# Kernel optimization log

Hardware: AMD Instinct MI355X
Metric: run time of the kernel (lower is better)

The kernel has to match this reference:

```python
import jax, jax.numpy as jnp
import numpy as np

BS, T, D, H = 2500, 400, 16, 32  # nodes(batch), time steps, input_dim, hidden_dim


def _xavier(key, shape):
    fan_in, fan_out = shape[0], shape[1]
    lim = np.sqrt(6.0 / (fan_in + fan_out)).astype(np.float32)
    return jax.random.uniform(key, shape, jnp.float32, -lim, lim)


def setup_inputs() -> dict:
    key = jax.random.key(0)
    ks = jax.random.split(key, 6)
    x = jax.random.normal(ks[0], (BS, T, D), jnp.float32)
    # dense adjacency over the batch/node dim, scaled small like a normalized river-network adjacency
    adj = jax.random.normal(ks[1], (BS, BS), jnp.float32) * 0.01
    return {
        "x": x,
        "adj": adj,
        "W_ih": _xavier(ks[2], (D, 4 * H)),
        "W_hh": _xavier(ks[3], (H, 4 * H)),
        "b": jnp.zeros((4 * H,), jnp.float32),
        "W_q": _xavier(ks[4], (H, H)),
        "b_q": jnp.zeros((H,), jnp.float32),
        "W_d": _xavier(ks[5], (H, 1)),
        "b_d": jnp.zeros((1,), jnp.float32),
    }


def reference(x, adj, W_ih, W_hh, b, W_q, b_q, W_d, b_d):
    # RGCN_Multi.forward_task0 (eval mode: dropouts are identity).
    HS = W_q.shape[0]
    bs = x.shape[0]

    def step(carry, x_t):
        h, c = carry  # [bs, HS] each
        gates = x_t @ W_ih + h @ W_hh + b  # [bs, 4*HS]
        i_t = jax.nn.sigmoid(gates[:, :HS])
        f_t = jax.nn.sigmoid(gates[:, HS:2 * HS])
        g_t = jnp.tanh(gates[:, 2 * HS:3 * HS])
        o_t = jax.nn.sigmoid(gates[:, 3 * HS:])
        q_t = jnp.tanh(h @ W_q + b_q)          # [bs, HS]
        c = f_t * (c + adj @ q_t) + i_t * g_t  # graph aggregation fused into cell state
        h = o_t * jnp.tanh(c)
        return (h, c), h

    h0 = jnp.zeros((bs, HS), x.dtype)
    (_, _), hs = jax.lax.scan(step, (h0, h0), jnp.swapaxes(x, 0, 1))  # hs: [T, bs, HS]
    hidden_seq = jnp.swapaxes(hs, 0, 1)  # [bs, T, HS]
    return hidden_seq @ W_d + b_d        # Task0Module dense head -> [bs, T, 1]
```

## Files before the change

### kernel.cpp

```cpp
#include <hip/hip_runtime.h>
#include <hip/hip_bf16.h>

#define BSN   2500
#define TT    400
#define DIN   16
#define HS    32
#define G4    128
#define NBLK  157
#define NTHR  512
#define ROWS  16
#define MPAD  (NBLK * ROWS)
#define KPAD  2528
#define NCHUNK 79
#define ADJW  2536
#define HPAD  36
#define FLAGSTRIDE 16

#define REGUS   (NCHUNK * 512)

#define WS_FLAGS_OFF  0
#define WS_ADJ_OFF    16384
#define WS_ADJ_BYTES  ((size_t)MPAD * KPAD * 2)
#define WS_QT_OFF     (WS_ADJ_OFF + WS_ADJ_BYTES)
#define QT_SLICE      ((size_t)HS * KPAD)
#define WS_NEED_RING  (WS_QT_OFF + (size_t)TT * QT_SLICE * 2)

typedef __attribute__((ext_vector_type(8))) __bf16 bf16x8;
typedef __attribute__((ext_vector_type(4))) float floatx4;
typedef unsigned short ushort_t;
typedef unsigned long long u64_t;

__device__ __forceinline__ float sigmoid_fast(float v) {
    return 1.0f / (1.0f + __expf(-v));
}
__device__ __forceinline__ float tanh_fast(float v) {
    float e = __expf(2.0f * v);
    return 1.0f - 2.0f / (e + 1.0f);
}
__device__ __forceinline__ ushort_t f2bf(float f) {
    union { float f; unsigned u; } x; x.f = f;
    unsigned r = x.u + 0x7fffu + ((x.u >> 16) & 1u);
    return (ushort_t)(r >> 16);
}

__global__ void sentinel(float* __restrict__ out, int n) {
    int i = blockIdx.x * blockDim.x + threadIdx.x;
    if (i < n) out[i] = 12345.0f;
}

__global__ void prep(const float* __restrict__ adj, ushort_t* __restrict__ adj_bf,
                     ushort_t* __restrict__ qT, unsigned* __restrict__ flags) {
    const size_t idx0 = (size_t)blockIdx.x * blockDim.x + threadIdx.x;
    const size_t stride = (size_t)gridDim.x * blockDim.x;
    const size_t total = (size_t)MPAD * KPAD;
    for (size_t idx = idx0; idx < total; idx += stride) {
        int r = (int)(idx / KPAD);
        int k = (int)(idx - (size_t)r * KPAD);
        float v = (r < BSN && k < BSN) ? adj[(size_t)r * BSN + k] : 0.0f;
        adj_bf[idx] = f2bf(v);
    }
    for (size_t idx = idx0; idx < 2 * QT_SLICE; idx += stride) qT[idx] = 0;
    if (idx0 < NBLK * FLAGSTRIDE) flags[idx0] = 0;
}

#define QLOAD(p) __hip_atomic_load((p), __ATOMIC_RELAXED, __HIP_MEMORY_SCOPE_AGENT)

template<int NC>
__device__ __forceinline__ void p2_frag(const ushort_t* __restrict__ arow,
                                        const ushort_t* __restrict__ q0,
                                        const ushort_t* __restrict__ q1,
                                        const int cbeg,
                                        floatx4& acc0, floatx4& acc1) {
    bf16x8 b0[NC], b1[NC];
#pragma unroll
    for (int i = 0; i < NC; i++) {
        b0[i] = *(const bf16x8*)(q0 + (size_t)(cbeg + i) * 512);
        b1[i] = *(const bf16x8*)(q1 + (size_t)(cbeg + i) * 512);
    }
#pragma unroll
    for (int i = 0; i < NC; i++) {
        bf16x8 av = *(const bf16x8*)(arow + (cbeg + i) * 32);
        acc0 = __builtin_amdgcn_mfma_f32_16x16x32_bf16(av, b0[i], acc0, 0, 0, 0);
        acc1 = __builtin_amdgcn_mfma_f32_16x16x32_bf16(av, b1[i], acc1, 0, 0, 0);
    }
}

template<bool RING>
__global__ void __launch_bounds__(NTHR, 2) rgcn_main(
    const float* __restrict__ x,
    const float* __restrict__ W_ih,
    const float* __restrict__ W_hh,
    const float* __restrict__ bias,
    const float* __restrict__ W_q,
    const float* __restrict__ b_q,
    const float* __restrict__ W_d,
    const float* __restrict__ b_d,
    const ushort_t* __restrict__ adj_bf,
    ushort_t* __restrict__ qT,
    unsigned* __restrict__ flags,
    float* __restrict__ out)
{
    const int tid  = threadIdx.x;
    const int blk  = blockIdx.x;
    const int base = blk * ROWS;
    const int wv   = tid >> 6;
    const int lane = tid & 63;

    __shared__ __align__(16) ushort_t adj_lds[ROWS * ADJW];
    __shared__ __align__(16) float x_lds[ROWS][DIN];
    __shared__ __align__(16) float h_lds[ROWS][HPAD];
    __shared__ __align__(16) float c_lds[ROWS][HPAD];
    __shared__ __align__(16) float q_lds[ROWS][HPAD];
    __shared__ __align__(16) float wq_lds[HS][HS];
    __shared__ __align__(16) float out_lds[ROWS][16];
    __shared__ float gates_lds[ROWS][G4];
    __shared__ float part[2][7][2][16][16];

    const int u2 = tid & 63;
    float wih0[DIN], wih1[DIN], whh0[HS], whh1[HS];
#pragma unroll
    for (int k = 0; k < DIN; k++) {
        wih0[k] = W_ih[k*G4 + u2]; wih1[k] = W_ih[k*G4 + u2 + 64];
        asm volatile("" : "+v"(wih0[k]), "+v"(wih1[k]));
    }
#pragma unroll
    for (int k = 0; k < HS; k++) {
        whh0[k] = W_hh[k*G4 + u2]; whh1[k] = W_hh[k*G4 + u2 + 64];
        asm volatile("" : "+v"(whh0[k]), "+v"(whh1[k]));
    }
    const float bu0 = bias[u2], bu1 = bias[u2 + 64];

    const int hq = tid & 31;
    const int nq = tid >> 5;
    const float bqv = b_q[hq];
    const float wdv = W_d[hq];
    const float bdv = b_d[0];
    float c_reg = 0.0f;

    int cbeg = 0, nch = 0;
    if (wv >= 1 && wv <= 3)      { cbeg = (wv - 1) * 12;      nch = 12; }
    else if (wv >= 4 && wv <= 6) { cbeg = 36 + (wv - 4) * 11; nch = 11; }
    else if (wv == 7)            { cbeg = 69;                 nch = 10; }
    const int pollbase = 2 * cbeg;
    const int pollcnt  = (wv == 0) ? 0
                       : ((2 * (cbeg + nch) < NBLK ? 2 * (cbeg + nch) : NBLK) - pollbase);
    const unsigned* pollf = flags + (size_t)(pollbase + lane) * FLAGSTRIDE;
    const bool dopoll = (wv >= 1) && (lane < pollcnt);

    int xnode = -1, xk = lane & 15;
    if (wv >= 1 && lane < 32)                   xnode = 2*wv + (lane >> 4);
    else if ((wv == 1 || wv == 2) && lane < 48) xnode = wv - 1;
    const int xgn = base + xnode;
    const bool xok = (xnode >= 0) && (xgn < BSN);

    {
        const int n16_per_row = KPAD / 8;
        for (int i = tid; i < ROWS * n16_per_row; i += NTHR) {
            int r = i / n16_per_row, o = i - r * n16_per_row;
            ((uint4*)(adj_lds + r * ADJW))[o] =
                ((const uint4*)(adj_bf + (size_t)(base + r) * KPAD))[o];
        }
    }
    for (int i = tid; i < HS * HS; i += NTHR) (&wq_lds[0][0])[i] = W_q[i];
    for (int i = tid; i < ROWS * HPAD; i += NTHR) {
        (&h_lds[0][0])[i] = 0.0f;
        (&c_lds[0][0])[i] = 0.0f;
    }
    __syncthreads();

    auto do_gates = [&](int nn) {
        float a0 = bu0, a1 = bu1;
#pragma unroll
        for (int k4 = 0; k4 < DIN/4; k4++) {
            float4 xv = *(const float4*)&x_lds[nn][k4*4];
            a0 = fmaf(xv.x, wih0[k4*4+0], a0); a1 = fmaf(xv.x, wih1[k4*4+0], a1);
            a0 = fmaf(xv.y, wih0[k4*4+1], a0); a1 = fmaf(xv.y, wih1[k4*4+1], a1);
            a0 = fmaf(xv.z, wih0[k4*4+2], a0); a1 = fmaf(xv.z, wih1[k4*4+2], a1);
            a0 = fmaf(xv.w, wih0[k4*4+3], a0); a1 = fmaf(xv.w, wih1[k4*4+3], a1);
        }
#pragma unroll
        for (int k4 = 0; k4 < HS/4; k4++) {
            float4 hv = *(const float4*)&h_lds[nn][k4*4];
            a0 = fmaf(hv.x, whh0[k4*4+0], a0); a1 = fmaf(hv.x, whh1[k4*4+0], a1);
            a0 = fmaf(hv.y, whh0[k4*4+1], a0); a1 = fmaf(hv.y, whh1[k4*4+1], a1);
            a0 = fmaf(hv.z, whh0[k4*4+2], a0); a1 = fmaf(hv.z, whh1[k4*4+2], a1);
            a0 = fmaf(hv.w, whh0[k4*4+3], a0); a1 = fmaf(hv.w, whh1[k4*4+3], a1);
        }
        gates_lds[nn][u2]      = sigmoid_fast(a0);
        gates_lds[nn][u2 + 64] = (u2 < HS) ? tanh_fast(a1) : sigmoid_fast(a1);
    };

    if constexpr (RING) {
        float xreg = xok ? x[(size_t)xgn * (TT*DIN) + xk] : 0.0f;

        const int pc    = blk >> 1;
        const int phalf = blk & 1;
        const int preg  = lane >> 5;
        const int pidx  = lane & 31;
        const int ph    = (pidx & 15) + 16 * preg;
        const int pln0  = (pidx >> 4) * 8;

        for (int t = 0; t < TT; t++) {
            const unsigned phase = (unsigned)(t + 1);
            const ushort_t* qslice = qT + (size_t)t * QT_SLICE;

            {
                float a = bqv;
#pragma unroll
                for (int k4 = 0; k4 < HS/4; k4++) {
                    float4 hv = *(const float4*)&h_lds[nq][k4*4];
                    a = fmaf(hv.x, wq_lds[k4*4+0][hq], a);
                    a = fmaf(hv.y, wq_lds[k4*4+1][hq], a);
                    a = fmaf(hv.z, wq_lds[k4*4+2][hq], a);
                    a = fmaf(hv.w, wq_lds[k4*4+3][hq], a);
                }
                q_lds[nq][hq] = tanh_fast(a);
            }
            __syncthreads();

            if (wv == 0) {
                unsigned d[4];
#pragma unroll
                for (int j = 0; j < 4; j++) {
                    const int n0 = pln0 + 2*j;
                    d[j] = (unsigned)f2bf(q_lds[n0][ph])
                         | ((unsigned)f2bf(q_lds[n0 + 1][ph]) << 16);
                }
                u64_t v0 = (u64_t)d[0] | ((u64_t)d[1] << 32);
                u64_t v1 = (u64_t)d[2] | ((u64_t)d[3] << 32);
                u64_t* dst = (u64_t*)((ushort_t*)qslice + (size_t)preg * REGUS
                                      + (size_t)pc * 512 + phalf * 256 + pidx * 8);
                __hip_atomic_store(dst,     v0, __ATOMIC_RELAXED, __HIP_MEMORY_SCOPE_AGENT);
                __hip_atomic_store(dst + 1, v1, __ATOMIC_RELAXED, __HIP_MEMORY_SCOPE_AGENT);
                asm volatile("s_waitcnt vmcnt(0)" ::: "memory");
                if (lane == 0) {
                    __hip_atomic_store(flags + blk * FLAGSTRIDE, phase,
                                       __ATOMIC_RELAXED, __HIP_MEMORY_SCOPE_AGENT);
                }
            } else {
                if (xnode >= 0) {
                    x_lds[xnode][xk] = xok ? xreg : 0.0f;
                    const int tn = (t + 1 < TT) ? (t + 1) : (TT - 1);
                    if (xok) xreg = x[(size_t)xgn * (TT*DIN) + (size_t)tn * DIN + xk];
                }
                do_gates(2*wv);
                do_gates(2*wv + 1);
                if (wv <= 2) do_gates(wv - 1);
            }

            if (dopoll) {
                while (QLOAD(pollf) < phase) {}
            }

            if (wv >= 1) {
                floatx4 acc0 = {0.f,0.f,0.f,0.f}, acc1 = {0.f,0.f,0.f,0.f};
                const int mcol = lane & 15;
                const int kb   = lane >> 4;
                const ushort_t* arow = adj_lds + mcol * ADJW + kb*8;
                const ushort_t* q0 = qslice + (size_t)lane * 8;
                const ushort_t* q1 = qslice + (size_t)REGUS + (size_t)lane * 8;
                if (wv <= 3)      p2_frag<12>(arow, q0, q1, cbeg, acc0, acc1);
                else if (wv <= 6) p2_frag<11>(arow, q0, q1, cbeg, acc0, acc1);
                else              p2_frag<10>(arow, q0, q1, cbeg, acc0, acc1);
#pragma unroll
                for (int r = 0; r < 4; r++) {
                    part[t & 1][wv - 1][0][kb*4 + r][mcol] = acc0[r];
                    part[t & 1][wv - 1][1][kb*4 + r][mcol] = acc1[r];
                }
            }
            __syncthreads();

            {
                const int ntile = hq >> 4, col = hq & 15;
                float agg = 0.0f;
#pragma unroll
                for (int j = 0; j < 7; j++) agg += part[t & 1][j][ntile][nq][col];
                float iv = gates_lds[nq][hq];
                float fv = gates_lds[nq][HS + hq];
                float gv = gates_lds[nq][2*HS + hq];
                float ov = gates_lds[nq][3*HS + hq];
                float cv = fv * (c_reg + agg) + iv * gv;
                float hvv = ov * tanh_fast(cv);
                c_reg = cv;
                h_lds[nq][hq] = hvv;
                float p = hvv * wdv;
                p += __shfl_xor(p, 16);
                p += __shfl_xor(p, 8);
                p += __shfl_xor(p, 4);
                p += __shfl_xor(p, 2);
                p += __shfl_xor(p, 1);
                if (hq == 0) out_lds[nq][t & 15] = p + bdv;
            }

            if ((t & 15) == 15) {
                __syncthreads();
                if (wv == 7) {
                    const int node = lane >> 2, qtr = lane & 3;
                    const int gn = base + node;
                    if (gn < BSN) {
                        *(float4*)(out + (size_t)gn * TT + (t - 15) + qtr * 4) =
                            *(const float4*)&out_lds[node][qtr * 4];
                    }
                }
            }
        }
    } else {
        for (int t = 0; t < TT; t++) {
            const unsigned phase = (unsigned)(t + 1);
            ushort_t* qbuf = qT + (size_t)(t & 1) * QT_SLICE;

            {
                float a = bqv;
#pragma unroll
                for (int k4 = 0; k4 < HS/4; k4++) {
                    float4 hv = *(const float4*)&h_lds[nq][k4*4];
                    a = fmaf(hv.x, wq_lds[k4*4+0][hq], a);
                    a = fmaf(hv.y, wq_lds[k4*4+1][hq], a);
                    a = fmaf(hv.z, wq_lds[k4*4+2][hq], a);
                    a = fmaf(hv.w, wq_lds[k4*4+3][hq], a);
                }
                q_lds[nq][hq] = tanh_fast(a);
            }
            __syncthreads();

            if (tid < 256) {
                const int h0 = tid >> 3;
                const int pr = tid & 7;
                unsigned val = (unsigned)f2bf(q_lds[2*pr][h0])
                             | ((unsigned)f2bf(q_lds[2*pr + 1][h0]) << 16);
                unsigned* p = (unsigned*)(qbuf + (size_t)h0 * KPAD + base) + pr;
                __hip_atomic_store(p, val, __ATOMIC_RELAXED, __HIP_MEMORY_SCOPE_AGENT);
            }
            if (lane < 32) {
                const int node = 2*wv + (lane >> 4), k = lane & 15;
                const int gn = base + node;
                x_lds[node][k] = (gn < BSN) ? x[(size_t)gn * (TT*DIN) + (size_t)t*DIN + k] : 0.0f;
            }
            do_gates(2*wv);
            do_gates(2*wv + 1);
            asm volatile("s_waitcnt vmcnt(0)" ::: "memory");
            __syncthreads();
            if (tid == 0) {
                __hip_atomic_store(flags + blk * FLAGSTRIDE, phase,
                                   __ATOMIC_RELAXED, __HIP_MEMORY_SCOPE_AGENT);
            }
            if (tid < NBLK) {
                const unsigned* f = flags + tid * FLAGSTRIDE;
                while (QLOAD(f) < phase) {}
            }
            __syncthreads();

            {
                floatx4 acc0 = {0.f,0.f,0.f,0.f}, acc1 = {0.f,0.f,0.f,0.f};
                const int mcol = lane & 15;
                const int kb   = lane >> 4;
                const ushort_t* arow = adj_lds + mcol * ADJW + kb*8;
                const u64_t* q0 = (const u64_t*)(qbuf + (size_t)mcol        * KPAD) + kb*2;
                const u64_t* q1 = (const u64_t*)(qbuf + (size_t)(mcol + 16) * KPAD) + kb*2;
                const int cb2 = wv * 10;
                const int ce2 = (cb2 + 10 < NCHUNK) ? cb2 + 10 : NCHUNK;
                for (int c = cb2; c < ce2; c++) {
                    bf16x8 av = *(const bf16x8*)(arow + c*32);
                    union { u64_t u[2]; bf16x8 v; } b0, b1;
                    b0.u[0] = QLOAD(q0 + c*8);
                    b0.u[1] = QLOAD(q0 + c*8 + 1);
                    b1.u[0] = QLOAD(q1 + c*8);
                    b1.u[1] = QLOAD(q1 + c*8 + 1);
                    acc0 = __builtin_amdgcn_mfma_f32_16x16x32_bf16(av, b0.v, acc0, 0, 0, 0);
                    acc1 = __builtin_amdgcn_mfma_f32_16x16x32_bf16(av, b1.v, acc1, 0, 0, 0);
                }
                part[wv >> 2][(wv & 3) + ((wv >> 2) ? 3 : 0)][0][kb*4 + 0][mcol] = acc0[0];
#pragma unroll
                for (int r = 0; r < 4; r++) {
                    part[0][wv % 7][0][kb*4 + r][mcol] = 0.0f;
                }
                float* pw = &part[0][0][0][0][0] + (size_t)wv * 2 * 16 * 16;
#pragma unroll
                for (int r = 0; r < 4; r++) {
                    pw[(0*16 + kb*4 + r) * 16 + mcol] = acc0[r];
                    pw[(1*16 + kb*4 + r) * 16 + mcol] = acc1[r];
                }
            }
            __syncthreads();

            {
                const int ntile = hq >> 4, col = hq & 15;
                float agg = 0.0f;
                const float* pbase = &part[0][0][0][0][0];
#pragma unroll
                for (int w = 0; w < 8; w++) {
                    agg += pbase[(size_t)w * 2 * 16 * 16 + (ntile*16 + nq) * 16 + col];
                }
                float iv = gates_lds[nq][hq];
                float fv = gates_lds[nq][HS + hq];
                float gv = gates_lds[nq][2*HS + hq];
                float ov = gates_lds[nq][3*HS + hq];
                float cv = fv * (c_lds[nq][hq] + agg) + iv * gv;
                float hv = ov * tanh_fast(cv);
                c_lds[nq][hq] = cv;
                h_lds[nq][hq] = hv;
                float p = hv * wdv;
                p += __shfl_xor(p, 16);
                p += __shfl_xor(p, 8);
                p += __shfl_xor(p, 4);
                p += __shfl_xor(p, 2);
                p += __shfl_xor(p, 1);
                if (hq == 0) {
                    int gn = base + nq;
                    if (gn < BSN) out[(size_t)gn * TT + t] = p + bdv;
                }
            }
            __syncthreads();
        }
    }
}

extern "C" void kernel_launch(void* const* d_in, const int* in_sizes, int n_in,
                              void* d_out, int out_size, void* d_ws, size_t ws_size,
                              hipStream_t stream) {
    const float* x    = (const float*)d_in[0];
    const float* adj  = (const float*)d_in[1];
    const float* W_ih = (const float*)d_in[2];
    const float* W_hh = (const float*)d_in[3];
    const float* bias = (const float*)d_in[4];
    const float* W_q  = (const float*)d_in[5];
    const float* b_q  = (const float*)d_in[6];
    const float* W_d  = (const float*)d_in[7];
    const float* b_d  = (const float*)d_in[8];
    float* out = (float*)d_out;

    unsigned* flags = (unsigned*)((char*)d_ws + WS_FLAGS_OFF);
    ushort_t* adj_bf = (ushort_t*)((char*)d_ws + WS_ADJ_OFF);
    ushort_t* qT = (ushort_t*)((char*)d_ws + WS_QT_OFF);

    const bool ring = (ws_size >= WS_NEED_RING);

    hipLaunchKernelGGL(sentinel, dim3((out_size + 255) / 256), dim3(256), 0, stream,
                       out, out_size);
    hipLaunchKernelGGL(prep, dim3(2048), dim3(256), 0, stream, adj, adj_bf, qT, flags);

    const ushort_t* adj_bf_c = adj_bf;
    void* args[] = {
        (void*)&x, (void*)&W_ih, (void*)&W_hh, (void*)&bias, (void*)&W_q,
        (void*)&b_q, (void*)&W_d, (void*)&b_d, (void*)&adj_bf_c, (void*)&qT,
        (void*)&flags, (void*)&out
    };
    if (ring) {
        hipLaunchCooperativeKernel((void*)&rgcn_main<true>, dim3(NBLK), dim3(NTHR),
                                   args, 0, stream);
    } else {
        hipLaunchCooperativeKernel((void*)&rgcn_main<false>, dim3(NBLK), dim3(NTHR),
                                   args, 0, stream);
    }
}
```

Measured before the change: 1.831 ms.

## Store adjacency in MFMA fragment order, keep W_q in registers, move output flush

Rearranges the per-block adjacency tile in LDS into fragment-contiguous order, so each lane reads its bf16x8 operand from a contiguous 512-element chunk without a padded row stride. W_q columns are loaded into per-thread registers instead of LDS, removing LDS reads from the q projection. The periodic output flush moves from a separate barrier-guarded step at t%16==15 into the wave-0 idle slot at the next 16-step boundary, which drops one __syncthreads per 16 steps. Register pressure rises by 32 floats per thread under a 2-blocks-per-CU launch bound.

```diff
diff --git a/kernel.cpp b/kernel.cpp
--- a/kernel.cpp
+++ b/kernel.cpp
@@ -12,7 +12,6 @@
 #define MPAD  (NBLK * ROWS)
 #define KPAD  2528
 #define NCHUNK 79
-#define ADJW  2536
 #define HPAD  36
 #define FLAGSTRIDE 16
 
@@ -66,7 +65,7 @@
 #define QLOAD(p) __hip_atomic_load((p), __ATOMIC_RELAXED, __HIP_MEMORY_SCOPE_AGENT)
 
 template<int NC>
-__device__ __forceinline__ void p2_frag(const ushort_t* __restrict__ arow,
+__device__ __forceinline__ void p2_frag(const ushort_t* __restrict__ afrag,
                                         const ushort_t* __restrict__ q0,
                                         const ushort_t* __restrict__ q1,
                                         const int cbeg,
@@ -79,7 +78,7 @@
     }
 #pragma unroll
     for (int i = 0; i < NC; i++) {
-        bf16x8 av = *(const bf16x8*)(arow + (cbeg + i) * 32);
+        bf16x8 av = *(const bf16x8*)(afrag + (size_t)(cbeg + i) * 512);
         acc0 = __builtin_amdgcn_mfma_f32_16x16x32_bf16(av, b0[i], acc0, 0, 0, 0);
         acc1 = __builtin_amdgcn_mfma_f32_16x16x32_bf16(av, b1[i], acc1, 0, 0, 0);
     }
@@ -106,12 +105,11 @@
     const int wv   = tid >> 6;
     const int lane = tid & 63;
 
-    __shared__ __align__(16) ushort_t adj_lds[ROWS * ADJW];
+    __shared__ __align__(16) ushort_t adj_lds[NCHUNK * 512];
     __shared__ __align__(16) float x_lds[ROWS][DIN];
     __shared__ __align__(16) float h_lds[ROWS][HPAD];
     __shared__ __align__(16) float c_lds[ROWS][HPAD];
     __shared__ __align__(16) float q_lds[ROWS][HPAD];
-    __shared__ __align__(16) float wq_lds[HS][HS];
     __shared__ __align__(16) float out_lds[ROWS][16];
     __shared__ float gates_lds[ROWS][G4];
     __shared__ float part[2][7][2][16][16];
@@ -136,6 +134,13 @@
     const float wdv = W_d[hq];
     const float bdv = b_d[0];
     float c_reg = 0.0f;
+
+    float wqr[HS];
+#pragma unroll
+    for (int k = 0; k < HS; k++) {
+        wqr[k] = W_q[k*HS + hq];
+        asm volatile("" : "+v"(wqr[k]));
+    }
 
     int cbeg = 0, nch = 0;
     if (wv >= 1 && wv <= 3)      { cbeg = (wv - 1) * 12;      nch = 12; }
@@ -157,11 +162,11 @@
         const int n16_per_row = KPAD / 8;
         for (int i = tid; i < ROWS * n16_per_row; i += NTHR) {
             int r = i / n16_per_row, o = i - r * n16_per_row;
-            ((uint4*)(adj_lds + r * ADJW))[o] =
+            int c = o >> 2, kb = o & 3;
+            *(uint4*)(adj_lds + (size_t)c * 512 + (size_t)(kb * 16 + r) * 8) =
                 ((const uint4*)(adj_bf + (size_t)(base + r) * KPAD))[o];
         }
     }
-    for (int i = tid; i < HS * HS; i += NTHR) (&wq_lds[0][0])[i] = W_q[i];
     for (int i = tid; i < ROWS * HPAD; i += NTHR) {
         (&h_lds[0][0])[i] = 0.0f;
         (&c_lds[0][0])[i] = 0.0f;
@@ -190,6 +195,19 @@
         gates_lds[nn][u2 + 64] = (u2 < HS) ? tanh_fast(a1) : sigmoid_fast(a1);
     };
 
+    auto do_p1b = [&]() {
+        float a = bqv;
+#pragma unroll
+        for (int k4 = 0; k4 < HS/4; k4++) {
+            float4 hv = *(const float4*)&h_lds[nq][k4*4];
+            a = fmaf(hv.x, wqr[k4*4+0], a);
+            a = fmaf(hv.y, wqr[k4*4+1], a);
+            a = fmaf(hv.z, wqr[k4*4+2], a);
+            a = fmaf(hv.w, wqr[k4*4+3], a);
+        }
+        q_lds[nq][hq] = tanh_fast(a);
+    };
+
     if constexpr (RING) {
         float xreg = xok ? x[(size_t)xgn * (TT*DIN) + xk] : 0.0f;
 
@@ -204,18 +222,7 @@
             const unsigned phase = (unsigned)(t + 1);
             const ushort_t* qslice = qT + (size_t)t * QT_SLICE;
 
-            {
-                float a = bqv;
-#pragma unroll
-                for (int k4 = 0; k4 < HS/4; k4++) {
-                    float4 hv = *(const float4*)&h_lds[nq][k4*4];
-                    a = fmaf(hv.x, wq_lds[k4*4+0][hq], a);
-                    a = fmaf(hv.y, wq_lds[k4*4+1][hq], a);
-                    a = fmaf(hv.z, wq_lds[k4*4+2][hq], a);
-                    a = fmaf(hv.w, wq_lds[k4*4+3][hq], a);
-                }
-                q_lds[nq][hq] = tanh_fast(a);
-            }
+            do_p1b();
             __syncthreads();
 
             if (wv == 0) {
@@ -237,6 +244,14 @@
                     __hip_atomic_store(flags + blk * FLAGSTRIDE, phase,
                                        __ATOMIC_RELAXED, __HIP_MEMORY_SCOPE_AGENT);
                 }
+                if (t >= 16 && (t & 15) == 0) {
+                    const int node = lane >> 2, qtr = lane & 3;
+                    const int gn = base + node;
+                    if (gn < BSN) {
+                        *(float4*)(out + (size_t)gn * TT + (t - 16) + qtr * 4) =
+                            *(const float4*)&out_lds[node][qtr * 4];
+                    }
+                }
             } else {
                 if (xnode >= 0) {
                     x_lds[xnode][xk] = xok ? xreg : 0.0f;
@@ -256,12 +271,12 @@
                 floatx4 acc0 = {0.f,0.f,0.f,0.f}, acc1 = {0.f,0.f,0.f,0.f};
                 const int mcol = lane & 15;
                 const int kb   = lane >> 4;
-                const ushort_t* arow = adj_lds + mcol * ADJW + kb*8;
+                const ushort_t* afrag = adj_lds + (size_t)lane * 8;
                 const ushort_t* q0 = qslice + (size_t)lane * 8;
                 const ushort_t* q1 = qslice + (size_t)REGUS + (size_t)lane * 8;
-                if (wv <= 3)      p2_frag<12>(arow, q0, q1, cbeg, acc0, acc1);
-                else if (wv <= 6) p2_frag<11>(arow, q0, q1, cbeg, acc0, acc1);
-                else              p2_frag<10>(arow, q0, q1, cbeg, acc0, acc1);
+                if (wv <= 3)      p2_frag<12>(afrag, q0, q1, cbeg, acc0, acc1);
+                else if (wv <= 6) p2_frag<11>(afrag, q0, q1, cbeg, acc0, acc1);
+                else              p2_frag<10>(afrag, q0, q1, cbeg, acc0, acc1);
 #pragma unroll
                 for (int r = 0; r < 4; r++) {
                     part[t & 1][wv - 1][0][kb*4 + r][mcol] = acc0[r];
@@ -291,17 +306,14 @@
                 p += __shfl_xor(p, 1);
                 if (hq == 0) out_lds[nq][t & 15] = p + bdv;
             }
-
-            if ((t & 15) == 15) {
-                __syncthreads();
-                if (wv == 7) {
-                    const int node = lane >> 2, qtr = lane & 3;
-                    const int gn = base + node;
-                    if (gn < BSN) {
-                        *(float4*)(out + (size_t)gn * TT + (t - 15) + qtr * 4) =
-                            *(const float4*)&out_lds[node][qtr * 4];
-                    }
-                }
+        }
+        __syncthreads();
+        if (wv == 0) {
+            const int node = lane >> 2, qtr = lane & 3;
+            const int gn = base + node;
+            if (gn < BSN) {
+                *(float4*)(out + (size_t)gn * TT + (TT - 16) + qtr * 4) =
+                    *(const float4*)&out_lds[node][qtr * 4];
             }
         }
     } else {
@@ -309,18 +321,7 @@
             const unsigned phase = (unsigned)(t + 1);
             ushort_t* qbuf = qT + (size_t)(t & 1) * QT_SLICE;
 
-            {
-                float a = bqv;
-#pragma unroll
-                for (int k4 = 0; k4 < HS/4; k4++) {
-                    float4 hv = *(const float4*)&h_lds[nq][k4*4];
-                    a = fmaf(hv.x, wq_lds[k4*4+0][hq], a);
-                    a = fmaf(hv.y, wq_lds[k4*4+1][hq], a);
-                    a = fmaf(hv.z, wq_lds[k4*4+2][hq], a);
-                    a = fmaf(hv.w, wq_lds[k4*4+3][hq], a);
-                }
-                q_lds[nq][hq] = tanh_fast(a);
-            }
+            do_p1b();
             __syncthreads();
 
             if (tid < 256) {
@@ -354,13 +355,13 @@
                 floatx4 acc0 = {0.f,0.f,0.f,0.f}, acc1 = {0.f,0.f,0.f,0.f};
                 const int mcol = lane & 15;
                 const int kb   = lane >> 4;
-                const ushort_t* arow = adj_lds + mcol * ADJW + kb*8;
+                const ushort_t* afrag = adj_lds + (size_t)lane * 8;
                 const u64_t* q0 = (const u64_t*)(qbuf + (size_t)mcol        * KPAD) + kb*2;
                 const u64_t* q1 = (const u64_t*)(qbuf + (size_t)(mcol + 16) * KPAD) + kb*2;
                 const int cb2 = wv * 10;
                 const int ce2 = (cb2 + 10 < NCHUNK) ? cb2 + 10 : NCHUNK;
                 for (int c = cb2; c < ce2; c++) {
-                    bf16x8 av = *(const bf16x8*)(arow + c*32);
+                    bf16x8 av = *(const bf16x8*)(afrag + (size_t)c * 512);
                     union { u64_t u[2]; bf16x8 v; } b0, b1;
                     b0.u[0] = QLOAD(q0 + c*8);
                     b0.u[1] = QLOAD(q0 + c*8 + 1);
@@ -368,11 +369,6 @@
                     b1.u[1] = QLOAD(q1 + c*8 + 1);
                     acc0 = __builtin_amdgcn_mfma_f32_16x16x32_bf16(av, b0.v, acc0, 0, 0, 0);
                     acc1 = __builtin_amdgcn_mfma_f32_16x16x32_bf16(av, b1.v, acc1, 0, 0, 0);
-                }
-                part[wv >> 2][(wv & 3) + ((wv >> 2) ? 3 : 0)][0][kb*4 + 0][mcol] = acc0[0];
-#pragma unroll
-                for (int r = 0; r < 4; r++) {
-                    part[0][wv % 7][0][kb*4 + r][mcol] = 0.0f;
                 }
                 float* pw = &part[0][0][0][0][0] + (size_t)wv * 2 * 16 * 16;
 #pragma unroll
```

After: 1.796 ms. About the same (-1.9%).
